# Kernel optimization log

Measured on AMD Instinct MI355X. Metric: run time of the kernel, lower is better.

The kernel has to match this reference:

```python
import jax, jax.numpy as jnp
import numpy as np

L, D, H = 5, 300, 600          # num_layers, emb_dim, mlp hidden (2*emb_dim)
NG = 512                       # number of graphs in the batch
ATOM_V, BOND_V = 64, 8         # per-feature vocab sizes
BN_EPS = 1e-5


def _bn(h, gamma, beta):
    # BatchNorm1d in training mode (batch statistics, biased variance)
    mu = h.mean(axis=0)
    var = ((h - mu) ** 2).mean(axis=0)
    return (h - mu) * jax.lax.rsqrt(var + BN_EPS) * gamma + beta


def reference(x, edge_index, edge_attr, batch,
              atom_emb, bond_emb, eps, W1, b1, g1, be1, W2, b2, g2, be2,
              head_w, head_b):
    N = x.shape[0]
    # AtomEncoder: sum of per-feature embeddings, feature f uses rows [f*ATOM_V, (f+1)*ATOM_V)
    h = atom_emb[x + jnp.arange(x.shape[1]) * ATOM_V].sum(axis=1)          # [N, D]
    e_idx = edge_attr + jnp.arange(edge_attr.shape[1]) * BOND_V            # [E, 3]
    src, dst = edge_index[0], edge_index[1]
    for l in range(L):
        e = bond_emb[l][e_idx].sum(axis=1)                                 # per-layer BondEncoder [E, D]
        msg = jax.nn.relu(h[src] + e)                                      # gather + message [E, D]
        agg = jax.ops.segment_sum(msg, dst, num_segments=N)                # scatter-add [N, D]
        z = (1.0 + eps[l]) * h + agg                                       # GIN update
        z = jax.nn.relu(_bn(z @ W1[l] + b1[l], g1[l], be1[l]))             # mlp: Lin+BN+ReLU
        z = z @ W2[l] + b2[l]                                              # mlp: Lin
        h = _bn(z, g2[l], be2[l])                                          # outer BatchNorm
        if l < L - 1:                                                      # no ReLU on last layer
            h = jax.nn.relu(h)
    hg = jax.ops.segment_sum(h, batch, num_segments=NG)                    # global_add_pool [NG, D]
    mu = hg.mean(axis=1, keepdims=True)                                    # GroupNorm(1, D, affine=False)
    var = ((hg - mu) ** 2).mean(axis=1, keepdims=True)
    hg = (hg - mu) * jax.lax.rsqrt(var + BN_EPS)
    return hg @ head_w + head_b                                            # [NG, num_tasks]


def setup_inputs() -> dict:
    key = jax.random.key(0)
    ks = jax.random.split(key, 12)
    N, E = 20000, 320000
    x = jax.random.randint(ks[0], (N, 9), 0, ATOM_V)
    edge_index = jax.random.randint(ks[1], (2, E), 0, N)
    edge_attr = jax.random.randint(ks[2], (E, 3), 0, BOND_V)
    batch = jnp.sort(jax.random.randint(ks[3], (N,), 0, NG))
    f = lambda k, shp: jax.random.normal(k, shp, dtype=jnp.float32) * 0.02
    return dict(
        x=x, edge_index=edge_index, edge_attr=edge_attr, batch=batch,
        atom_emb=f(ks[4], (9 * ATOM_V, D)),
        bond_emb=f(ks[5], (L, 3 * BOND_V, D)),
        eps=jnp.zeros((L,), jnp.float32),
        W1=f(ks[6], (L, D, H)), b1=jnp.zeros((L, H), jnp.float32),
        g1=jnp.ones((L, H), jnp.float32), be1=jnp.zeros((L, H), jnp.float32),
        W2=f(ks[7], (L, H, D)), b2=jnp.zeros((L, D), jnp.float32),
        g2=jnp.ones((L, D), jnp.float32), be2=jnp.zeros((L, D), jnp.float32),
        head_w=f(ks[8], (D, 1)), head_b=jnp.zeros((1,), jnp.float32),
    )
```

## Files before the change

kernel.cpp:

```cpp
#include <hip/hip_runtime.h>
#include <cstddef>
#include <cstdint>

#define DD 300
#define HH 600
#define LL 5
#define NGG 512
#define KP1 320
#define KP2 608
#define NP1 640
#define NP2 384
#define Z2LD 304
#define CLD 304

typedef unsigned short u16;
typedef _Float16 f16x8 __attribute__((ext_vector_type(8)));
typedef float f32x4 __attribute__((ext_vector_type(4)));

__device__ __forceinline__ u16 f2h(float v)
{
    _Float16 h = (_Float16)v; u16 u; __builtin_memcpy(&u, &h, 2); return u;
}
__device__ __forceinline__ float h2f(u16 u)
{
    _Float16 h; __builtin_memcpy(&h, &u, 2); return (float)h;
}

__device__ __forceinline__ void g2l16(const void* g, void* l)
{
    __builtin_amdgcn_global_load_lds(
        (const __attribute__((address_space(1))) void*)g,
        (__attribute__((address_space(3))) void*)l, 16, 0, 0);
}

__global__ __launch_bounds__(320) void atom_kernel(const int* __restrict__ x,
    const float* __restrict__ emb, u16* __restrict__ z2, int N)
{
    __shared__ int xi[9];
    int n = blockIdx.x;
    int t = threadIdx.x;
    if (t < 9) xi[t] = x[n * 9 + t] + t * 64;
    __syncthreads();
    if (t >= Z2LD) return;
    if (t >= DD) { z2[(size_t)n * Z2LD + t] = 0; return; }
    float s = 0.f;
#pragma unroll
    for (int f = 0; f < 9; ++f) s += emb[(size_t)xi[f] * DD + t];
    z2[(size_t)n * Z2LD + t] = f2h(s);
}

__global__ void csr_count(const int* __restrict__ dst, int E, int* __restrict__ cnt)
{
    int i = blockIdx.x * blockDim.x + threadIdx.x;
    int stride = gridDim.x * blockDim.x;
    for (; i < E; i += stride) atomicAdd(&cnt[dst[i]], 1);
}

__global__ __launch_bounds__(1024) void scan_kernel(const int* __restrict__ cnt,
    int* __restrict__ rowptr, int n)
{
    __shared__ int buf[1024];
    int t = threadIdx.x;
    int carry = 0;
    for (int base = 0; base < n; base += 1024) {
        int v = (base + t < n) ? cnt[base + t] : 0;
        buf[t] = v;
        __syncthreads();
        for (int off = 1; off < 1024; off <<= 1) {
            int x = (t >= off) ? buf[t - off] : 0;
            __syncthreads();
            buf[t] += x;
            __syncthreads();
        }
        if (base + t < n) rowptr[base + t] = buf[t] - v + carry;
        int total = buf[1023];
        __syncthreads();
        carry += total;
    }
    if (t == 0) rowptr[n] = carry;
}

__global__ void csr_fill(const int* __restrict__ src, const int* __restrict__ dst,
    const int* __restrict__ ea, const int* __restrict__ rowptr,
    int* __restrict__ cursor, int* __restrict__ rec, int E)
{
    int i = blockIdx.x * blockDim.x + threadIdx.x;
    int stride = gridDim.x * blockDim.x;
    for (; i < E; i += stride) {
        int d = dst[i];
        int pos = rowptr[d] + atomicAdd(&cursor[d], 1);
        int code = ea[i * 3] | (ea[i * 3 + 1] << 3) | (ea[i * 3 + 2] << 6);
        rec[pos] = src[i] | (code << 20);
    }
}

__global__ __launch_bounds__(320) void combo_build(const float* __restrict__ bond,
    u16* __restrict__ combo)
{
    int blk = blockIdx.x;
    int l = blk >> 9, code = blk & 511;
    int t = threadIdx.x;
    if (t >= CLD) return;
    u16 val = 0;
    if (t < DD) {
        const float* bl = bond + (size_t)l * 24 * DD;
        float v = bl[(size_t)(code & 7) * DD + t]
                + bl[(size_t)(8 + ((code >> 3) & 7)) * DD + t]
                + bl[(size_t)(16 + (code >> 6)) * DD + t];
        val = f2h(v);
    }
    combo[(size_t)blk * CLD + t] = val;
}

__global__ __launch_bounds__(256) void w_prep_t(const float* __restrict__ W,
    int K, int N, int KPp, int NPp, int ktiles, u16* __restrict__ Thi)
{
    __shared__ float tile[64][65];
    int ntiles = NPp >> 6;
    int blk = blockIdx.x;
    int l = blk / (ktiles * ntiles);
    int rem = blk % (ktiles * ntiles);
    int k0 = (rem / ntiles) << 6;
    int n0 = (rem % ntiles) << 6;
    int tn = threadIdx.x & 63;
    int tg = threadIdx.x >> 6;
    const float* Wl = W + (size_t)l * K * N;
    for (int kk = tg; kk < 64; kk += 4) {
        int gk = k0 + kk, gn = n0 + tn;
        tile[kk][tn] = (gk < K && gn < N) ? Wl[(size_t)gk * N + gn] : 0.f;
    }
    __syncthreads();
    for (int nn = tg; nn < 64; nn += 4) {
        int gn = n0 + nn, gk = k0 + tn;
        if (gk < KPp) {
            size_t o = ((size_t)l * NPp + gn) * KPp + gk;
            Thi[o] = f2h(tile[tn][nn]);
        }
    }
}

template <bool AFF>
__global__ __launch_bounds__(256) void agg_kernel(const u16* __restrict__ z2,
    const int* __restrict__ rec, const int* __restrict__ rowptr,
    const u16* __restrict__ combo_l,
    const float* __restrict__ sc, const float* __restrict__ sh,
    const float* __restrict__ eps, int l, u16* __restrict__ A1)
{
    __shared__ float part[6][304];
    int n = blockIdx.x;
    int t = threadIdx.x;
    int eo = t / 38, ch = t - eo * 38;
    int d0 = ch * 8;
    int beg = rowptr[n], end = rowptr[n + 1];

    if (eo < 6) {
        float acc[8] = {0.f, 0.f, 0.f, 0.f, 0.f, 0.f, 0.f, 0.f};
        float scv[8], shv[8];
        if (AFF) {
#pragma unroll
            for (int j = 0; j < 8; ++j) { scv[j] = sc[d0 + j]; shv[j] = sh[d0 + j]; }
        }
        int i = beg + eo;
        for (; i + 6 < end; i += 12) {
            int r0 = rec[i], r1 = rec[i + 6];
            uint4 hv0 = *(const uint4*)(z2 + (size_t)(r0 & 0xFFFFF) * Z2LD + d0);
            uint4 cv0 = *(const uint4*)(combo_l + (size_t)(((unsigned)r0) >> 20) * CLD + d0);
            uint4 hv1 = *(const uint4*)(z2 + (size_t)(r1 & 0xFFFFF) * Z2LD + d0);
            uint4 cv1 = *(const uint4*)(combo_l + (size_t)(((unsigned)r1) >> 20) * CLD + d0);
            const u16* hp0 = (const u16*)&hv0; const u16* cp0 = (const u16*)&cv0;
            const u16* hp1 = (const u16*)&hv1; const u16* cp1 = (const u16*)&cv1;
#pragma unroll
            for (int j = 0; j < 8; ++j) {
                float h0 = h2f(hp0[j]), h1 = h2f(hp1[j]);
                if (AFF) {
                    h0 = fmaxf(fmaf(h0, scv[j], shv[j]), 0.f);
                    h1 = fmaxf(fmaf(h1, scv[j], shv[j]), 0.f);
                }
                acc[j] += fmaxf(h0 + h2f(cp0[j]), 0.f) + fmaxf(h1 + h2f(cp1[j]), 0.f);
            }
        }
        for (; i < end; i += 6) {
            int r0 = rec[i];
            uint4 hv0 = *(const uint4*)(z2 + (size_t)(r0 & 0xFFFFF) * Z2LD + d0);
            uint4 cv0 = *(const uint4*)(combo_l + (size_t)(((unsigned)r0) >> 20) * CLD + d0);
            const u16* hp0 = (const u16*)&hv0; const u16* cp0 = (const u16*)&cv0;
#pragma unroll
            for (int j = 0; j < 8; ++j) {
                float h0 = h2f(hp0[j]);
                if (AFF) h0 = fmaxf(fmaf(h0, scv[j], shv[j]), 0.f);
                acc[j] += fmaxf(h0 + h2f(cp0[j]), 0.f);
            }
        }
        *(float4*)&part[eo][d0]     = *(const float4*)&acc[0];
        *(float4*)&part[eo][d0 + 4] = *(const float4*)&acc[4];
    }
    __syncthreads();

    if (t < 152) {
        float se = 1.0f + eps[l];
        int d = t * 2;
#pragma unroll
        for (int k = 0; k < 2; ++k) {
            int dd = d + k;
            float s = part[0][dd] + part[1][dd] + part[2][dd]
                    + part[3][dd] + part[4][dd] + part[5][dd];
            float hn = h2f(z2[(size_t)n * Z2LD + dd]);
            if (AFF) hn = fmaxf(fmaf(hn, sc[dd], sh[dd]), 0.f);
            A1[(size_t)n * KP1 + dd] = f2h(fmaf(se, hn, s));
        }
    } else if (t < 160) {
        int d = 304 + (t - 152) * 2;
        A1[(size_t)n * KP1 + d] = 0;
        A1[(size_t)n * KP1 + d + 1] = 0;
    }
}

template <bool FUSE>
__global__ __launch_bounds__(512, 4) void gemm_rs(
    const u16* __restrict__ Af, int lda,
    const u16* __restrict__ Bw,
    const float* __restrict__ bias,
    const float* __restrict__ scA, const float* __restrict__ shA,
    u16* __restrict__ O, int ldc, int M, int N, int ksteps,
    float* __restrict__ cs, float* __restrict__ csq, int ncol, int nwg)
{
    __shared__ __align__(16) u16 As[2][4][128][8];
    __shared__ __align__(16) u16 Bs[3][4][128][8];
    __shared__ float sc_s[FUSE ? 640 : 1], sh_s[FUSE ? 640 : 1];

    const int t = threadIdx.x;
    const int lane = t & 63, w = t >> 6;
    const int l15 = lane & 15, l4 = lane >> 4;
    const int wr = w >> 2, wc = w & 3;

    int orig = blockIdx.x;
    int q8 = nwg >> 3, r8 = nwg & 7;
    int xcd = orig & 7, i8 = orig >> 3;
    int wgid = (xcd < r8 ? xcd * (q8 + 1) : r8 * (q8 + 1) + (xcd - r8) * q8) + i8;
    const int col0 = (wgid % ncol) * 128;
    const int row0 = (wgid / ncol) * 128;

    if (FUSE) {
        for (int c = t; c < lda; c += 512) { sc_s[c] = scA[c]; sh_s[c] = shA[c]; }
    }

    const int arow = t >> 2;
    const int kg   = t & 3;
    const int k8   = kg * 8;
    const u16* aptr = Af + (size_t)(row0 + arow) * lda + k8;

    const int bkg = w >> 1, bch = w & 1;
    const u16* bptr = Bw + (size_t)(col0 + bch * 64 + lane) * lda + bkg * 8;

    auto loadAv = [&](int ks, uint4& pv) {
        pv = *(const uint4*)(aptr + ks * 32);
    };
    auto issueB = [&](int ks, int buf) {
        g2l16(bptr + ks * 32, &Bs[buf][bkg][bch * 64][0]);
    };
    auto writeAv = [&](int ks, int buf, uint4& pv) {
        if (FUSE) {
            const u16* hp = (const u16*)&pv;
            u16 oh[8];
#pragma unroll
            for (int j = 0; j < 8; ++j) {
                int c = ks * 32 + k8 + j;
                float xv = fmaxf(fmaf(h2f(hp[j]), sc_s[c], sh_s[c]), 0.f);
                oh[j] = f2h(xv);
            }
            *(uint4*)&As[buf][kg][arow][0] = *(const uint4*)oh;
        } else {
            *(uint4*)&As[buf][kg][arow][0] = pv;
        }
    };

    f32x4 acc[4][2];
#pragma unroll
    for (int i = 0; i < 4; ++i)
#pragma unroll
        for (int j = 0; j < 2; ++j) acc[i][j] = (f32x4){0.f, 0.f, 0.f, 0.f};

    uint4 pvA, pvB;
    __syncthreads();
    loadAv(0, pvA);
    issueB(0, 0);
    issueB(1, 1);
    loadAv(1, pvB);
    writeAv(0, 0, pvA);
    asm volatile("s_waitcnt vmcnt(2) lgkmcnt(0)" ::: "memory");
    __builtin_amdgcn_s_barrier();

    int cur = 0, rb = 0, tb = 2;
    auto body = [&](int ks, uint4& hold, uint4& fill) {
        const bool more1 = (ks + 1 < ksteps), more2 = (ks + 2 < ksteps);
        if (more2) { loadAv(ks + 2, fill); issueB(ks + 2, tb); }

        f16x8 a[4], b[2];
#pragma unroll
        for (int i = 0; i < 4; ++i) {
            int r = wr * 64 + i * 16 + l15;
            a[i] = *(const f16x8*)As[cur][l4][r];
        }
#pragma unroll
        for (int i = 0; i < 2; ++i) {
            int c = wc * 32 + i * 16 + l15;
            b[i] = *(const f16x8*)Bs[rb][l4][c];
        }
#pragma unroll
        for (int mi = 0; mi < 4; ++mi)
#pragma unroll
            for (int ni = 0; ni < 2; ++ni)
                acc[mi][ni] = __builtin_amdgcn_mfma_f32_16x16x32_f16(a[mi], b[ni], acc[mi][ni], 0, 0, 0);

        if (more1) {
            writeAv(ks + 1, cur ^ 1, hold);
            if (more2) asm volatile("s_waitcnt vmcnt(2) lgkmcnt(0)" ::: "memory");
            else       asm volatile("s_waitcnt vmcnt(0) lgkmcnt(0)" ::: "memory");
            __builtin_amdgcn_s_barrier();
        }
        cur ^= 1;
        rb = (rb == 2) ? 0 : rb + 1;
        tb = (tb == 2) ? 0 : tb + 1;
    };
    int ks = 0;
    for (; ks + 1 < ksteps; ks += 2) { body(ks, pvB, pvA); body(ks + 1, pvA, pvB); }
    if (ks < ksteps) body(ks, pvB, pvA);

    float colS[2] = {0.f, 0.f}, colQ[2] = {0.f, 0.f};
#pragma unroll
    for (int ni = 0; ni < 2; ++ni) {
        int gc = col0 + wc * 32 + ni * 16 + l15;
        float bb = (gc < N) ? bias[gc] : 0.f;
#pragma unroll
        for (int mi = 0; mi < 4; ++mi)
#pragma unroll
            for (int r = 0; r < 4; ++r) {
                int gr = row0 + wr * 64 + mi * 16 + l4 * 4 + r;
                if (gr >= M) continue;
                if (gc < N) {
                    float val = acc[mi][ni][r] + bb;
                    O[(size_t)gr * ldc + gc] = f2h(val);
                    colS[ni] += val;
                    colQ[ni] += val * val;
                } else if (gc < ldc) {
                    O[(size_t)gr * ldc + gc] = 0;
                }
            }
    }
#pragma unroll
    for (int ni = 0; ni < 2; ++ni) {
        float s = colS[ni], q = colQ[ni];
        s += __shfl_xor(s, 16); s += __shfl_xor(s, 32);
        q += __shfl_xor(q, 16); q += __shfl_xor(q, 32);
        int gc = col0 + wc * 32 + ni * 16 + l15;
        if (l4 == 0 && gc < N) {
            atomicAdd(&cs[gc], s);
            atomicAdd(&csq[gc], q);
        }
    }
}

__global__ void bn_fin(float* __restrict__ cs, float* __restrict__ csq,
                       const float* __restrict__ g, const float* __restrict__ be,
                       float* __restrict__ scale, float* __restrict__ shift,
                       int cols, int colspad, float invn)
{
    int c = blockIdx.x * blockDim.x + threadIdx.x;
    if (c >= colspad) return;
    if (c >= cols) { scale[c] = 0.f; shift[c] = 0.f; return; }
    float mu = cs[c] * invn;
    float var = csq[c] * invn - mu * mu;
    float rs = rsqrtf(var + 1e-5f);
    float sc = rs * g[c];
    scale[c] = sc;
    shift[c] = be[c] - mu * sc;
    cs[c] = 0.f;
    csq[c] = 0.f;
}

__global__ __launch_bounds__(320) void pool_kernel(const u16* __restrict__ z2,
    const int* __restrict__ batch, int N,
    const float* __restrict__ sc, const float* __restrict__ sh,
    float* __restrict__ hg)
{
    int g = blockIdx.x;
    int lo = 0, hi = N;
    while (lo < hi) { int mid = (lo + hi) >> 1; if (batch[mid] < g) lo = mid + 1; else hi = mid; }
    int start = lo;
    hi = N;
    while (lo < hi) { int mid = (lo + hi) >> 1; if (batch[mid] <= g) lo = mid + 1; else hi = mid; }
    int end = lo;
    int d = threadIdx.x;
    if (d >= DD) return;
    float s = 0.f;
    for (int i = start; i < end; ++i) s += h2f(z2[(size_t)i * Z2LD + d]);
    hg[(size_t)g * DD + d] = sc[d] * s + (float)(end - start) * sh[d];
}

__global__ __launch_bounds__(256) void head_kernel(const float* __restrict__ hg,
    const float* __restrict__ w, const float* __restrict__ b, float* __restrict__ out)
{
    __shared__ float red[256];
    int g = blockIdx.x, t = threadIdx.x;
    const float* row = hg + (size_t)g * DD;
    float v0 = (t < DD) ? row[t] : 0.f;
    float v1 = (t + 256 < DD) ? row[t + 256] : 0.f;

    red[t] = v0 + v1;
    __syncthreads();
    for (int o = 128; o > 0; o >>= 1) { if (t < o) red[t] += red[t + o]; __syncthreads(); }
    float mean = red[0] * (1.f / (float)DD);
    __syncthreads();

    red[t] = v0 * v0 + v1 * v1;
    __syncthreads();
    for (int o = 128; o > 0; o >>= 1) { if (t < o) red[t] += red[t + o]; __syncthreads(); }
    float var = red[0] * (1.f / (float)DD) - mean * mean;
    float rs = rsqrtf(var + 1e-5f);
    __syncthreads();

    float d0 = (t < DD) ? (v0 - mean) * rs * w[t] : 0.f;
    float d1 = (t + 256 < DD) ? (v1 - mean) * rs * w[t + 256] : 0.f;
    red[t] = d0 + d1;
    __syncthreads();
    for (int o = 128; o > 0; o >>= 1) { if (t < o) red[t] += red[t + o]; __syncthreads(); }
    if (t == 0) out[g] = red[0] + b[0];
}

extern "C" void kernel_launch(void* const* d_in, const int* in_sizes, int n_in,
                              void* d_out, int out_size, void* d_ws, size_t ws_size,
                              hipStream_t stream)
{
    (void)n_in; (void)out_size; (void)ws_size;
    const int*   x         = (const int*)  d_in[0];
    const int*   edge_idx  = (const int*)  d_in[1];
    const int*   edge_attr = (const int*)  d_in[2];
    const int*   batch     = (const int*)  d_in[3];
    const float* atom_emb  = (const float*)d_in[4];
    const float* bond_emb  = (const float*)d_in[5];
    const float* eps       = (const float*)d_in[6];
    const float* W1        = (const float*)d_in[7];
    const float* b1        = (const float*)d_in[8];
    const float* g1        = (const float*)d_in[9];
    const float* be1       = (const float*)d_in[10];
    const float* W2        = (const float*)d_in[11];
    const float* b2        = (const float*)d_in[12];
    const float* g2        = (const float*)d_in[13];
    const float* be2       = (const float*)d_in[14];
    const float* head_w    = (const float*)d_in[15];
    const float* head_b    = (const float*)d_in[16];

    const int NN = in_sizes[3];
    const int E  = in_sizes[1] / 2;
    const int gm = (NN + 127) / 128;
    const int mpad = gm * 128;
    const float invn = 1.f / (float)NN;

    char* p = (char*)d_ws;
    auto alloc = [&](size_t bytes) { char* r = p; p += (bytes + 255) & ~(size_t)255; return r; };

    u16* z2g    = (u16*)  alloc((size_t)NN * Z2LD * 2);
    u16* A1     = (u16*)  alloc((size_t)mpad * KP1 * 2);
    u16* Z1     = (u16*)  alloc((size_t)mpad * KP2 * 2);
    u16* W1T    = (u16*)  alloc((size_t)LL * NP1 * KP1 * 2);
    u16* W2T    = (u16*)  alloc((size_t)LL * NP2 * KP2 * 2);
    u16* combo  = (u16*)  alloc((size_t)LL * 512 * CLD * 2);
    float* hg   = (float*)alloc((size_t)NGG * DD * 4);
    float* cs   = (float*)alloc(HH * 4 * 2);
    float* csq  = cs + HH;
    float* sc1  = (float*)alloc(640 * 4);
    float* sh1  = (float*)alloc(640 * 4);
    float* sc2  = (float*)alloc(Z2LD * 4);
    float* sh2  = (float*)alloc(Z2LD * 4);
    int* cnt    = (int*)  alloc((size_t)NN * 4 * 2);
    int* cursor = cnt + NN;
    int* rowptr = (int*)  alloc((size_t)(NN + 1) * 4);
    int* rec    = (int*)  alloc((size_t)E * 4);

    const int* src = edge_idx;
    const int* dst = edge_idx + E;

    hipMemsetAsync(cnt, 0, (size_t)NN * 2 * sizeof(int), stream);
    hipMemsetAsync(cs, 0, (size_t)HH * 2 * sizeof(float), stream);
    csr_count<<<512, 256, 0, stream>>>(dst, E, cnt);
    scan_kernel<<<1, 1024, 0, stream>>>(cnt, rowptr, NN);
    csr_fill<<<512, 256, 0, stream>>>(src, dst, edge_attr, rowptr, cursor, rec, E);
    combo_build<<<LL * 512, 320, 0, stream>>>(bond_emb, combo);
    w_prep_t<<<LL * (KP1 / 64) * (NP1 / 64), 256, 0, stream>>>(
        W1, DD, HH, KP1, NP1, KP1 / 64, W1T);
    w_prep_t<<<LL * ((KP2 + 63) / 64) * (NP2 / 64), 256, 0, stream>>>(
        W2, HH, DD, KP2, NP2, (KP2 + 63) / 64, W2T);
    atom_kernel<<<NN, 320, 0, stream>>>(x, atom_emb, z2g, NN);

    const int nwg1 = (NP1 / 128) * gm;
    const int nwg2 = (NP2 / 128) * gm;
    for (int l = 0; l < LL; ++l) {
        const u16* combo_l = combo + (size_t)l * 512 * CLD;
        if (l == 0)
            agg_kernel<false><<<NN, 256, 0, stream>>>(z2g, rec, rowptr, combo_l,
                nullptr, nullptr, eps, l, A1);
        else
            agg_kernel<true><<<NN, 256, 0, stream>>>(z2g, rec, rowptr, combo_l,
                sc2, sh2, eps, l, A1);

        gemm_rs<false><<<nwg1, 512, 0, stream>>>(
            A1, KP1, W1T + (size_t)l * NP1 * KP1,
            b1 + (size_t)l * HH, nullptr, nullptr,
            Z1, KP2, NN, HH, KP1 / 32, cs, csq, NP1 / 128, nwg1);

        bn_fin<<<(KP2 + 255) / 256, 256, 0, stream>>>(cs, csq, g1 + (size_t)l * HH,
            be1 + (size_t)l * HH, sc1, sh1, HH, KP2, invn);

        gemm_rs<true><<<nwg2, 512, 0, stream>>>(
            Z1, KP2, W2T + (size_t)l * NP2 * KP2,
            b2 + (size_t)l * DD, sc1, sh1,
            z2g, Z2LD, NN, DD, KP2 / 32, cs, csq, NP2 / 128, nwg2);

        bn_fin<<<(Z2LD + 255) / 256, 256, 0, stream>>>(cs, csq, g2 + (size_t)l * DD,
            be2 + (size_t)l * DD, sc2, sh2, DD, Z2LD, invn);
    }

    pool_kernel<<<NGG, 320, 0, stream>>>(z2g, batch, NN, sc2, sh2, hg);
    head_kernel<<<NGG, 256, 0, stream>>>(hg, head_w, head_b, (float*)d_out);
}
```

Baseline: 787.0 us.

## Use packed fp16 math in edge aggregation and deepen GEMM A-prefetch pipeline

The aggregation kernel now applies the BN affine, ReLU, bond-embedding add and message ReLU on packed half2 vectors, widening to fp32 only for accumulation. This halves the per-element conversion and ALU work in the gather loop, at the cost of doing those intermediate ops in fp16. The GEMM now prefetches A tiles three k-steps ahead into registers using a third buffer, rotating A, B and C and adjusting the vmcnt waits. This is meant to hide more global-load latency for A, but it uses extra registers.

```diff
diff --git a/kernel.cpp b/kernel.cpp
--- a/kernel.cpp
+++ b/kernel.cpp
@@ -15,6 +15,7 @@
 
 typedef unsigned short u16;
 typedef _Float16 f16x8 __attribute__((ext_vector_type(8)));
+typedef _Float16 h2 __attribute__((ext_vector_type(2)));
 typedef float f32x4 __attribute__((ext_vector_type(4)));
 
 __device__ __forceinline__ u16 f2h(float v)
@@ -155,10 +156,14 @@
 
     if (eo < 6) {
         float acc[8] = {0.f, 0.f, 0.f, 0.f, 0.f, 0.f, 0.f, 0.f};
-        float scv[8], shv[8];
+        h2 scp[4], shp[4];
+        const h2 zz = {(_Float16)0.f, (_Float16)0.f};
         if (AFF) {
 #pragma unroll
-            for (int j = 0; j < 8; ++j) { scv[j] = sc[d0 + j]; shv[j] = sh[d0 + j]; }
+            for (int j = 0; j < 4; ++j) {
+                scp[j] = (h2){(_Float16)sc[d0 + 2 * j], (_Float16)sc[d0 + 2 * j + 1]};
+                shp[j] = (h2){(_Float16)sh[d0 + 2 * j], (_Float16)sh[d0 + 2 * j + 1]};
+            }
         }
         int i = beg + eo;
         for (; i + 6 < end; i += 12) {
@@ -167,28 +172,33 @@
             uint4 cv0 = *(const uint4*)(combo_l + (size_t)(((unsigned)r0) >> 20) * CLD + d0);
             uint4 hv1 = *(const uint4*)(z2 + (size_t)(r1 & 0xFFFFF) * Z2LD + d0);
             uint4 cv1 = *(const uint4*)(combo_l + (size_t)(((unsigned)r1) >> 20) * CLD + d0);
-            const u16* hp0 = (const u16*)&hv0; const u16* cp0 = (const u16*)&cv0;
-            const u16* hp1 = (const u16*)&hv1; const u16* cp1 = (const u16*)&cv1;
-#pragma unroll
-            for (int j = 0; j < 8; ++j) {
-                float h0 = h2f(hp0[j]), h1 = h2f(hp1[j]);
+            const h2* hp0 = (const h2*)&hv0; const h2* cp0 = (const h2*)&cv0;
+            const h2* hp1 = (const h2*)&hv1; const h2* cp1 = (const h2*)&cv1;
+#pragma unroll
+            for (int j = 0; j < 4; ++j) {
+                h2 a0 = hp0[j], a1 = hp1[j];
                 if (AFF) {
-                    h0 = fmaxf(fmaf(h0, scv[j], shv[j]), 0.f);
-                    h1 = fmaxf(fmaf(h1, scv[j], shv[j]), 0.f);
+                    a0 = __builtin_elementwise_max(a0 * scp[j] + shp[j], zz);
+                    a1 = __builtin_elementwise_max(a1 * scp[j] + shp[j], zz);
                 }
-                acc[j] += fmaxf(h0 + h2f(cp0[j]), 0.f) + fmaxf(h1 + h2f(cp1[j]), 0.f);
+                h2 m0 = __builtin_elementwise_max(a0 + cp0[j], zz);
+                h2 m1 = __builtin_elementwise_max(a1 + cp1[j], zz);
+                acc[2 * j]     += (float)m0.x + (float)m1.x;
+                acc[2 * j + 1] += (float)m0.y + (float)m1.y;
             }
         }
         for (; i < end; i += 6) {
             int r0 = rec[i];
             uint4 hv0 = *(const uint4*)(z2 + (size_t)(r0 & 0xFFFFF) * Z2LD + d0);
             uint4 cv0 = *(const uint4*)(combo_l + (size_t)(((unsigned)r0) >> 20) * CLD + d0);
-            const u16* hp0 = (const u16*)&hv0; const u16* cp0 = (const u16*)&cv0;
-#pragma unroll
-            for (int j = 0; j < 8; ++j) {
-                float h0 = h2f(hp0[j]);
-                if (AFF) h0 = fmaxf(fmaf(h0, scv[j], shv[j]), 0.f);
-                acc[j] += fmaxf(h0 + h2f(cp0[j]), 0.f);
+            const h2* hp0 = (const h2*)&hv0; const h2* cp0 = (const h2*)&cv0;
+#pragma unroll
+            for (int j = 0; j < 4; ++j) {
+                h2 a0 = hp0[j];
+                if (AFF) a0 = __builtin_elementwise_max(a0 * scp[j] + shp[j], zz);
+                h2 m0 = __builtin_elementwise_max(a0 + cp0[j], zz);
+                acc[2 * j]     += (float)m0.x;
+                acc[2 * j + 1] += (float)m0.y;
             }
         }
         *(float4*)&part[eo][d0]     = *(const float4*)&acc[0];
@@ -280,20 +290,23 @@
 #pragma unroll
         for (int j = 0; j < 2; ++j) acc[i][j] = (f32x4){0.f, 0.f, 0.f, 0.f};
 
-    uint4 pvA, pvB;
+    uint4 pvA, pvB, pvC;
     __syncthreads();
     loadAv(0, pvA);
     issueB(0, 0);
     issueB(1, 1);
     loadAv(1, pvB);
+    loadAv(2, pvC);
     writeAv(0, 0, pvA);
-    asm volatile("s_waitcnt vmcnt(2) lgkmcnt(0)" ::: "memory");
+    asm volatile("s_waitcnt vmcnt(3) lgkmcnt(0)" ::: "memory");
     __builtin_amdgcn_s_barrier();
 
     int cur = 0, rb = 0, tb = 2;
     auto body = [&](int ks, uint4& hold, uint4& fill) {
-        const bool more1 = (ks + 1 < ksteps), more2 = (ks + 2 < ksteps);
-        if (more2) { loadAv(ks + 2, fill); issueB(ks + 2, tb); }
+        const bool more1 = (ks + 1 < ksteps), more2 = (ks + 2 < ksteps),
+                   more3 = (ks + 3 < ksteps);
+        if (more2) issueB(ks + 2, tb);
+        if (more3) loadAv(ks + 3, fill);
 
         f16x8 a[4], b[2];
 #pragma unroll
@@ -314,17 +327,20 @@
 
         if (more1) {
             writeAv(ks + 1, cur ^ 1, hold);
-            if (more2) asm volatile("s_waitcnt vmcnt(2) lgkmcnt(0)" ::: "memory");
-            else       asm volatile("s_waitcnt vmcnt(0) lgkmcnt(0)" ::: "memory");
+            if (more3)      asm volatile("s_waitcnt vmcnt(3) lgkmcnt(0)" ::: "memory");
+            else if (more2) asm volatile("s_waitcnt vmcnt(2) lgkmcnt(0)" ::: "memory");
+            else            asm volatile("s_waitcnt vmcnt(0) lgkmcnt(0)" ::: "memory");
             __builtin_amdgcn_s_barrier();
         }
         cur ^= 1;
         rb = (rb == 2) ? 0 : rb + 1;
         tb = (tb == 2) ? 0 : tb + 1;
     };
-    int ks = 0;
-    for (; ks + 1 < ksteps; ks += 2) { body(ks, pvB, pvA); body(ks + 1, pvA, pvB); }
-    if (ks < ksteps) body(ks, pvB, pvA);
+    for (int k = 0; k < ksteps; k += 3) {
+        body(k, pvB, pvA);
+        if (k + 1 < ksteps) body(k + 1, pvC, pvB);
+        if (k + 2 < ksteps) body(k + 2, pvA, pvC);
+    }
 
     float colS[2] = {0.f, 0.f}, colQ[2] = {0.f, 0.f};
 #pragma unroll
```

New measurement: 727.6 us. 7.5% less time.
